# Performance work log

Hardware: AMD Instinct MI355X
Metric: run time of the kernel (lower is better)

## Reference

```python
import jax, jax.numpy as jnp
import numpy as np

WS = 7   # window_size
NH = 4   # num_heads


def setup_inputs() -> dict:
    key = jax.random.key(0)
    k0, k1 = jax.random.split(key, 2)
    dim = 384
    B, H, W = 8, 224, 224
    x = jax.random.normal(k0, (B, dim, H, W), dtype=jnp.float32)
    # torch nn.Linear stores weight as [out_features, in_features]
    qkv_w = jax.random.normal(k1, (3 * dim, dim), dtype=jnp.float32) * (dim ** -0.5)
    qkv_b = jnp.zeros((3 * dim,), dtype=jnp.float32)
    return {"x": x, "qkv_w": qkv_w, "qkv_b": qkv_b}


def reference(x, qkv_w, qkv_b):
    B, C, H, W = x.shape
    ws, nh = WS, NH
    hd = C // nh
    # NCHW -> NHWC
    x = jnp.transpose(x, (0, 2, 3, 1))
    pad_h = (-H) % ws
    pad_w = (-W) % ws
    x = jnp.pad(x, ((0, 0), (0, pad_h), (0, pad_w), (0, 0)))
    Hp, Wp = H + pad_h, W + pad_w
    # window partition -> [B*nWh*nWw, ws*ws, C]
    x = x.reshape(B, Hp // ws, ws, Wp // ws, ws, C)
    x = jnp.transpose(x, (0, 1, 3, 2, 4, 5)).reshape(-1, ws * ws, C)
    # QKV projection (torch Linear: x @ W.T + b)
    qkv = x @ qkv_w.T + qkv_b
    q, k, v = jnp.split(qkv, 3, axis=-1)

    def to_heads(t):  # [nW, ws*ws, C] -> [nW, nh, ws*ws, hd]
        return jnp.transpose(t.reshape(t.shape[0], ws * ws, nh, hd), (0, 2, 1, 3))

    q, k, v = to_heads(q), to_heads(k), to_heads(v)
    scale = jnp.asarray(hd, x.dtype) ** -0.5
    scores = jnp.einsum('wnqd,wnkd->wnqk', q * scale, k)
    attn = jax.nn.softmax(scores, axis=-1)
    out = jnp.einsum('wnqk,wnkd->wnqd', attn, v)
    # merge heads and reverse window partition
    out = jnp.transpose(out, (0, 2, 1, 3)).reshape(-1, ws * ws, C)
    out = out.reshape(B, Hp // ws, Wp // ws, ws, ws, C)
    out = jnp.transpose(out, (0, 1, 3, 2, 4, 5)).reshape(B, Hp, Wp, C)
    out = out[:, :H, :W, :]
    return jnp.transpose(out, (0, 3, 1, 2))
```

## Files before the change

kernel.cpp:

```cpp
#include <hip/hip_runtime.h>

typedef __attribute__((ext_vector_type(4))) float f32x4;
typedef __attribute__((ext_vector_type(8))) short s16x8;
typedef __attribute__((ext_vector_type(8))) unsigned short u16x8;

#define TOKS_PER_B 50176
#define CDIM 384
#define OCDIM 1152

__device__ __forceinline__ unsigned short f2bf(float f) {
  unsigned u = __builtin_bit_cast(unsigned, f);
  u += 0x7FFFu + ((u >> 16) & 1u);
  return (unsigned short)(u >> 16);
}
__device__ __forceinline__ unsigned cvt_pk(float lo, float hi) {
  unsigned r;
  asm("v_cvt_pk_bf16_f32 %0, %1, %2" : "=v"(r) : "v"(lo), "v"(hi));
  return r;
}

__global__ __launch_bounds__(256) void qkv_gemm(
    const float* __restrict__ x, const float* __restrict__ wq,
    const float* __restrict__ bias, unsigned short* __restrict__ qkv,
    long long t_base, int nwg) {
  __shared__ unsigned short As[128][32];
  __shared__ unsigned short Bs[128][32];
  const int tid  = threadIdx.x;
  const int lane = tid & 63, wv = tid >> 6;

  const int qq  = nwg >> 3, rr = nwg & 7;
  const int xcd = blockIdx.x & 7, pos = blockIdx.x >> 3;
  const int wgid = (xcd < rr ? xcd * (qq + 1) : rr * (qq + 1) + (xcd - rr) * qq) + pos;
  const int nb = wgid % 9, mb = wgid / 9;

  const long long t0 = t_base + (long long)mb * 128;
  const int b    = (int)(t0 / TOKS_PER_B);
  const int off0 = (int)(t0 - (long long)b * TOKS_PER_B);
  const float* xb = x + (size_t)b * CDIM * TOKS_PER_B + off0;
  const int n0 = nb * 128;
  const int ml = lane & 15, quad = lane >> 4;
  const int m_base = (wv & 1) * 64, n_base = (wv >> 1) * 64;

  const int tok  = tid & 127;
  const int kh   = (tid >> 7) << 4;
  const int keyA = (tok ^ (tok >> 2)) & 3;
  const int cA0  = kh >> 3;
  unsigned short* aw0 = &As[tok][((cA0 ^ keyA) << 3)];
  unsigned short* aw1 = &As[tok][(((cA0 + 1) ^ keyA) << 3)];
  const float* apk = xb + (size_t)kh * TOKS_PER_B + tok;

  const int bk4  = (tid & 7) * 4;
  const int bn   = tid >> 3;
  const int keyB = (bn ^ (bn >> 2)) & 3;
  const int bwoff = (((bk4 >> 3) ^ keyB) << 3) + (bk4 & 7);
  const float* wqp = wq + (size_t)(n0 + bn) * CDIM + bk4;

  const int keyR = (ml ^ (ml >> 2)) & 3;
  const int rq   = (quad ^ keyR) << 3;

  f32x4 acc[4][4] = {};

  for (int ks = 0; ks < 12; ++ks) {
    float va[16];
    #pragma unroll
    for (int i = 0; i < 16; ++i) va[i] = apk[(size_t)i * TOKS_PER_B];
    float4 vb[4];
    #pragma unroll
    for (int p = 0; p < 4; ++p) vb[p] = *(const float4*)(wqp + (size_t)p * 32 * CDIM);

    uint4 w;
    w.x = cvt_pk(va[0], va[1]);   w.y = cvt_pk(va[2], va[3]);
    w.z = cvt_pk(va[4], va[5]);   w.w = cvt_pk(va[6], va[7]);
    *(uint4*)aw0 = w;
    w.x = cvt_pk(va[8], va[9]);   w.y = cvt_pk(va[10], va[11]);
    w.z = cvt_pk(va[12], va[13]); w.w = cvt_pk(va[14], va[15]);
    *(uint4*)aw1 = w;
    #pragma unroll
    for (int p = 0; p < 4; ++p) {
      uint2 u;
      u.x = cvt_pk(vb[p].x, vb[p].y);
      u.y = cvt_pk(vb[p].z, vb[p].w);
      *(uint2*)&Bs[bn + p * 32][bwoff] = u;
    }
    __syncthreads();

    s16x8 af[4], bf[4];
    #pragma unroll
    for (int mi = 0; mi < 4; ++mi)
      af[mi] = __builtin_bit_cast(s16x8, *(const u16x8*)&As[m_base + mi * 16 + ml][rq]);
    #pragma unroll
    for (int ni = 0; ni < 4; ++ni)
      bf[ni] = __builtin_bit_cast(s16x8, *(const u16x8*)&Bs[n_base + ni * 16 + ml][rq]);
    #pragma unroll
    for (int mi = 0; mi < 4; ++mi)
      #pragma unroll
      for (int ni = 0; ni < 4; ++ni)
        acc[mi][ni] = __builtin_amdgcn_mfma_f32_16x16x32_bf16(af[mi], bf[ni], acc[mi][ni], 0, 0, 0);
    __syncthreads();

    apk += (size_t)32 * TOKS_PER_B;
    wqp += 32;
  }

  const long long mrow0 = (long long)mb * 128 + m_base;
  #pragma unroll
  for (int ni = 0; ni < 4; ++ni) {
    const int col = n0 + n_base + ni * 16 + ml;
    const float bv = bias[col];
    #pragma unroll
    for (int mi = 0; mi < 4; ++mi) {
      #pragma unroll
      for (int r = 0; r < 4; ++r) {
        const long long mrow = mrow0 + mi * 16 + quad * 4 + r;
        qkv[(size_t)mrow * OCDIM + col] = f2bf(acc[mi][ni][r] + bv);
      }
    }
  }
}

__global__ __launch_bounds__(64) void win_attn(
    const unsigned short* __restrict__ qkv, float* __restrict__ out,
    int win_base) {
  __shared__ unsigned short sh[64 * 72 + 96 * 72];
  unsigned short* P  = sh;
  unsigned short* Vt = sh + 64 * 72;
  const int lane = threadIdx.x;
  const int win  = win_base + blockIdx.x;
  const int head = blockIdx.y;
  const int b = win >> 10, hw = (win >> 5) & 31, ww = win & 31;
  const long long t00 = (long long)b * TOKS_PER_B + (long long)hw * 7 * 224 + ww * 7
                        - (long long)(win_base >> 5) * 1568;
  const unsigned short* base = qkv + t00 * OCDIM + head * 96;
  const int ml = lane & 15, quad = lane >> 4;

  for (int idx = lane; idx < 49 * 96; idx += 64) {
    const int pos = idx / 96, d = idx - pos * 96;
    const int r = pos / 7, cc = pos - r * 7;
    Vt[d * 72 + pos] = base[(size_t)(r * 224 + cc) * OCDIM + 768 + d];
  }
  for (int idx = lane; idx < 96 * 15; idx += 64) {
    const int d = idx / 15, j = 49 + (idx - d * 15);
    Vt[d * 72 + j] = 0;
  }

  s16x8 aq[4][3], bk[4][3];
  const s16x8 zf = {0, 0, 0, 0, 0, 0, 0, 0};
  #pragma unroll
  for (int mi = 0; mi < 4; ++mi) {
    const int pos = mi * 16 + ml;
    if (pos < 49) {
      const int r = pos / 7, cc = pos - r * 7;
      const unsigned short* rowp = base + (size_t)(r * 224 + cc) * OCDIM;
      #pragma unroll
      for (int ks = 0; ks < 3; ++ks) {
        aq[mi][ks] = __builtin_bit_cast(s16x8, *(const u16x8*)(rowp + ks * 32 + quad * 8));
        bk[mi][ks] = __builtin_bit_cast(s16x8, *(const u16x8*)(rowp + 384 + ks * 32 + quad * 8));
      }
    } else {
      #pragma unroll
      for (int ks = 0; ks < 3; ++ks) { aq[mi][ks] = zf; bk[mi][ks] = zf; }
    }
  }

  f32x4 sa[4][4] = {};
  #pragma unroll
  for (int ks = 0; ks < 3; ++ks)
    #pragma unroll
    for (int mi = 0; mi < 4; ++mi)
      #pragma unroll
      for (int ni = 0; ni < 4; ++ni)
        sa[mi][ni] = __builtin_amdgcn_mfma_f32_16x16x32_bf16(aq[mi][ks], bk[ni][ks], sa[mi][ni], 0, 0, 0);

  const float scale = 0.10206207261596577f;
  #pragma unroll
  for (int mi = 0; mi < 4; ++mi) {
    #pragma unroll
    for (int r = 0; r < 4; ++r) {
      float mx = -3.0e38f;
      #pragma unroll
      for (int ni = 0; ni < 4; ++ni)
        if (ni * 16 + ml < 49) mx = fmaxf(mx, sa[mi][ni][r]);
      mx = fmaxf(mx, __shfl_xor(mx, 1, 16));
      mx = fmaxf(mx, __shfl_xor(mx, 2, 16));
      mx = fmaxf(mx, __shfl_xor(mx, 4, 16));
      mx = fmaxf(mx, __shfl_xor(mx, 8, 16));
      float e[4], sum = 0.f;
      #pragma unroll
      for (int ni = 0; ni < 4; ++ni) {
        e[ni] = (ni * 16 + ml < 49) ? __expf((sa[mi][ni][r] - mx) * scale) : 0.f;
        sum += e[ni];
      }
      sum += __shfl_xor(sum, 1, 16);
      sum += __shfl_xor(sum, 2, 16);
      sum += __shfl_xor(sum, 4, 16);
      sum += __shfl_xor(sum, 8, 16);
      const float inv = 1.0f / sum;
      const int row = mi * 16 + quad * 4 + r;
      #pragma unroll
      for (int ni = 0; ni < 4; ++ni)
        P[row * 72 + ni * 16 + ml] = f2bf(e[ni] * inv);
    }
  }

  f32x4 oa[4][6] = {};
  #pragma unroll
  for (int ks = 0; ks < 2; ++ks) {
    s16x8 ap[4], bv[6];
    #pragma unroll
    for (int mi = 0; mi < 4; ++mi)
      ap[mi] = __builtin_bit_cast(s16x8, *(const u16x8*)&P[(mi * 16 + ml) * 72 + ks * 32 + quad * 8]);
    #pragma unroll
    for (int ni = 0; ni < 6; ++ni)
      bv[ni] = __builtin_bit_cast(s16x8, *(const u16x8*)&Vt[(ni * 16 + ml) * 72 + ks * 32 + quad * 8]);
    #pragma unroll
    for (int mi = 0; mi < 4; ++mi)
      #pragma unroll
      for (int ni = 0; ni < 6; ++ni)
        oa[mi][ni] = __builtin_amdgcn_mfma_f32_16x16x32_bf16(ap[mi], bv[ni], oa[mi][ni], 0, 0, 0);
  }

  float* O = (float*)sh;
  #pragma unroll
  for (int mi = 0; mi < 4; ++mi)
    #pragma unroll
    for (int r = 0; r < 4; ++r) {
      const int row = mi * 16 + quad * 4 + r;
      if (row < 49) {
        #pragma unroll
        for (int ni = 0; ni < 6; ++ni)
          O[row * 99 + ni * 16 + ml] = oa[mi][ni][r];
      }
    }
  const size_t obase = ((size_t)(b * CDIM + head * 96) * 224 + (size_t)hw * 7) * 224 + ww * 7;
  for (int idx = lane; idx < 49 * 96; idx += 64) {
    const int d = idx / 49, pos = idx - d * 49;
    const int r = pos / 7, cc = pos - r * 7;
    out[obase + ((size_t)d * 224 + r) * 224 + cc] = O[pos * 99 + d];
  }
}

extern "C" void kernel_launch(void* const* d_in, const int* in_sizes, int n_in,
                              void* d_out, int out_size, void* d_ws, size_t ws_size,
                              hipStream_t stream) {
  const float* x    = (const float*)d_in[0];
  const float* wq   = (const float*)d_in[1];
  const float* bias = (const float*)d_in[2];
  float* out = (float*)d_out;
  unsigned short* ws = (unsigned short*)d_ws;

  const long long UNIT_TOK = 6272;
  const size_t UNIT_BYTES = (size_t)UNIT_TOK * OCDIM * 2;
  int upc = (int)(ws_size / UNIT_BYTES);
  if (upc < 1) upc = 1;
  if (upc > 64) upc = 64;

  for (int u0 = 0; u0 < 64; u0 += upc) {
    const int units = (u0 + upc <= 64) ? upc : (64 - u0);
    const long long t_base = (long long)u0 * UNIT_TOK;
    const int toks = units * (int)UNIT_TOK;
    const int nwg = 9 * (toks / 128);
    qkv_gemm<<<dim3(nwg), dim3(256), 0, stream>>>(x, wq, bias, ws, t_base, nwg);
    dim3 g2(units * 128, 4);
    win_attn<<<g2, dim3(64), 0, stream>>>(ws, out, u0 * 128);
  }
}
```

Measured before the change: 2.549 ms.

## Write QKV directly in per-window-head layout with pre-transposed V

```diff
diff --git a/kernel.cpp b/kernel.cpp
--- a/kernel.cpp
+++ b/kernel.cpp
@@ -6,7 +6,11 @@
 
 #define TOKS_PER_B 50176
 #define CDIM 384
-#define OCDIM 1152
+
+#define REG_HW   15552
+#define QOFF     0
+#define KOFF     4704
+#define VTOFF    9408
 
 __device__ __forceinline__ unsigned short f2bf(float f) {
   unsigned u = __builtin_bit_cast(unsigned, f);
@@ -19,9 +23,20 @@
   return r;
 }
 
+__global__ __launch_bounds__(256) void pad_zero(unsigned short* __restrict__ ws, int total) {
+  const int i = blockIdx.x * 256 + threadIdx.x;
+  if (i >= total) return;
+  const int reg = i / 96, d = i - reg * 96;
+  unsigned short* p = ws + (size_t)reg * REG_HW + VTOFF + d * 64 + 49;
+  p[0] = 0;
+  unsigned* q = (unsigned*)(p + 1);
+  #pragma unroll
+  for (int j = 0; j < 7; ++j) q[j] = 0;
+}
+
 __global__ __launch_bounds__(256) void qkv_gemm(
     const float* __restrict__ x, const float* __restrict__ wq,
-    const float* __restrict__ bias, unsigned short* __restrict__ qkv,
+    const float* __restrict__ bias, unsigned short* __restrict__ ws,
     long long t_base, int nwg) {
   __shared__ unsigned short As[128][32];
   __shared__ unsigned short Bs[128][32];
@@ -29,8 +44,8 @@
   const int lane = tid & 63, wv = tid >> 6;
 
   const int qq  = nwg >> 3, rr = nwg & 7;
-  const int xcd = blockIdx.x & 7, pos = blockIdx.x >> 3;
-  const int wgid = (xcd < rr ? xcd * (qq + 1) : rr * (qq + 1) + (xcd - rr) * qq) + pos;
+  const int xcd = blockIdx.x & 7, posb = blockIdx.x >> 3;
+  const int wgid = (xcd < rr ? xcd * (qq + 1) : rr * (qq + 1) + (xcd - rr) * qq) + posb;
   const int nb = wgid % 9, mb = wgid / 9;
 
   const long long t0 = t_base + (long long)mb * 128;
@@ -41,135 +56,135 @@
   const int ml = lane & 15, quad = lane >> 4;
   const int m_base = (wv & 1) * 64, n_base = (wv >> 1) * 64;
 
-  const int tok  = tid & 127;
-  const int kh   = (tid >> 7) << 4;
-  const int keyA = (tok ^ (tok >> 2)) & 3;
-  const int cA0  = kh >> 3;
-  unsigned short* aw0 = &As[tok][((cA0 ^ keyA) << 3)];
-  unsigned short* aw1 = &As[tok][(((cA0 + 1) ^ keyA) << 3)];
-  const float* apk = xb + (size_t)kh * TOKS_PER_B + tok;
+  const int am   = tid & 31;
+  const int akq  = tid >> 5;
+  const int atok = am * 4;
+  const int aswr = (am >> 2) & 1;
+  const int awoff = (((akq >> 1) ^ (am & 3)) << 3) + (akq & 1) * 4;
+  const float* apk = xb + (size_t)(akq * 4) * TOKS_PER_B + atok;
 
   const int bk4  = (tid & 7) * 4;
   const int bn   = tid >> 3;
-  const int keyB = (bn ^ (bn >> 2)) & 3;
-  const int bwoff = (((bk4 >> 3) ^ keyB) << 3) + (bk4 & 7);
+  const int bswr = (bn >> 4) & 1;
+  const int bwoff = (((bk4 >> 3) ^ ((bn >> 2) & 3)) << 3) + (bk4 & 7);
   const float* wqp = wq + (size_t)(n0 + bn) * CDIM + bk4;
 
-  const int keyR = (ml ^ (ml >> 2)) & 3;
-  const int rq   = (quad ^ keyR) << 3;
+  const int rq = (quad ^ (ml >> 2)) << 3;
 
   f32x4 acc[4][4] = {};
+  f32x4 va[4]; f32x4 vb[4];
+  #pragma unroll
+  for (int p = 0; p < 4; ++p) va[p] = *(const f32x4*)(apk + (size_t)p * TOKS_PER_B);
+  #pragma unroll
+  for (int p = 0; p < 4; ++p) vb[p] = *(const f32x4*)(wqp + (size_t)p * 32 * CDIM);
 
   for (int ks = 0; ks < 12; ++ks) {
-    float va[16];
-    #pragma unroll
-    for (int i = 0; i < 16; ++i) va[i] = apk[(size_t)i * TOKS_PER_B];
-    float4 vb[4];
-    #pragma unroll
-    for (int p = 0; p < 4; ++p) vb[p] = *(const float4*)(wqp + (size_t)p * 32 * CDIM);
-
-    uint4 w;
-    w.x = cvt_pk(va[0], va[1]);   w.y = cvt_pk(va[2], va[3]);
-    w.z = cvt_pk(va[4], va[5]);   w.w = cvt_pk(va[6], va[7]);
-    *(uint4*)aw0 = w;
-    w.x = cvt_pk(va[8], va[9]);   w.y = cvt_pk(va[10], va[11]);
-    w.z = cvt_pk(va[12], va[13]); w.w = cvt_pk(va[14], va[15]);
-    *(uint4*)aw1 = w;
+    #pragma unroll
+    for (int t = 0; t < 4; ++t) {
+      uint2 u;
+      u.x = cvt_pk(va[0][t], va[1][t]);
+      u.y = cvt_pk(va[2][t], va[3][t]);
+      *(uint2*)&As[(atok + t) ^ aswr][awoff] = u;
+    }
     #pragma unroll
     for (int p = 0; p < 4; ++p) {
       uint2 u;
-      u.x = cvt_pk(vb[p].x, vb[p].y);
-      u.y = cvt_pk(vb[p].z, vb[p].w);
-      *(uint2*)&Bs[bn + p * 32][bwoff] = u;
+      u.x = cvt_pk(vb[p][0], vb[p][1]);
+      u.y = cvt_pk(vb[p][2], vb[p][3]);
+      *(uint2*)&Bs[(bn + 32 * p) ^ bswr][bwoff] = u;
     }
     __syncthreads();
-
+    if (ks < 11) {
+      apk += (size_t)32 * TOKS_PER_B;
+      wqp += 32;
+      #pragma unroll
+      for (int p = 0; p < 4; ++p) va[p] = *(const f32x4*)(apk + (size_t)p * TOKS_PER_B);
+      #pragma unroll
+      for (int p = 0; p < 4; ++p) vb[p] = *(const f32x4*)(wqp + (size_t)p * 32 * CDIM);
+    }
     s16x8 af[4], bf[4];
     #pragma unroll
     for (int mi = 0; mi < 4; ++mi)
-      af[mi] = __builtin_bit_cast(s16x8, *(const u16x8*)&As[m_base + mi * 16 + ml][rq]);
+      af[mi] = __builtin_bit_cast(s16x8, *(const u16x8*)&As[(m_base + mi * 16 + ml) ^ (mi & 1)][rq]);
     #pragma unroll
     for (int ni = 0; ni < 4; ++ni)
-      bf[ni] = __builtin_bit_cast(s16x8, *(const u16x8*)&Bs[n_base + ni * 16 + ml][rq]);
+      bf[ni] = __builtin_bit_cast(s16x8, *(const u16x8*)&Bs[(n_base + ni * 16 + ml) ^ (ni & 1)][rq]);
     #pragma unroll
     for (int mi = 0; mi < 4; ++mi)
       #pragma unroll
       for (int ni = 0; ni < 4; ++ni)
         acc[mi][ni] = __builtin_amdgcn_mfma_f32_16x16x32_bf16(af[mi], bf[ni], acc[mi][ni], 0, 0, 0);
     __syncthreads();
-
-    apk += (size_t)32 * TOKS_PER_B;
-    wqp += 32;
-  }
-
-  const long long mrow0 = (long long)mb * 128 + m_base;
+  }
+
+  int isV_[4]; size_t coff_[4]; float bv_[4];
   #pragma unroll
   for (int ni = 0; ni < 4; ++ni) {
-    const int col = n0 + n_base + ni * 16 + ml;
-    const float bv = bias[col];
+    const int colb = n0 + n_base + ni * 16;
+    const int sel  = colb / 384;
+    const int hd   = (colb - sel * 384) / 96;
+    const int db   = colb - sel * 384 - hd * 96;
+    bv_[ni]  = bias[colb + ml];
+    isV_[ni] = (sel == 2);
+    coff_[ni] = (size_t)hd * REG_HW +
+                (isV_[ni] ? (size_t)VTOFF + (size_t)(db + ml) * 64
+                          : (size_t)sel * 4704 + (size_t)(db + ml));
+  }
+  const unsigned tl00 = (unsigned)(mb * 128 + m_base + quad * 4);
+  #pragma unroll
+  for (int mi = 0; mi < 4; ++mi) {
+    #pragma unroll
+    for (int r = 0; r < 4; ++r) {
+      const unsigned tl = tl00 + mi * 16 + r;
+      const unsigned rl = tl / 224;
+      const unsigned cc = tl - rl * 224;
+      const unsigned wr = rl / 7, pr = rl - wr * 7;
+      const unsigned wc = cc / 7, pc = cc - wc * 7;
+      const size_t   wbase = (size_t)(wr * 32 + wc) * 4 * REG_HW;
+      const unsigned pos = pr * 7 + pc;
+      #pragma unroll
+      for (int ni = 0; ni < 4; ++ni) {
+        const unsigned short val = f2bf(acc[mi][ni][r] + bv_[ni]);
+        ws[wbase + coff_[ni] + (isV_[ni] ? (size_t)pos : (size_t)pos * 96)] = val;
+      }
+    }
+  }
+}
+
+__global__ __launch_bounds__(64) void win_attn(
+    const unsigned short* __restrict__ ws, float* __restrict__ out, int win_base) {
+  __shared__ float shraw[2450];
+  unsigned short* P = (unsigned short*)shraw;
+  float* O = shraw;
+  const int lane = threadIdx.x;
+  const int ml = lane & 15, quad = lane >> 4;
+  const int w = blockIdx.x, head = blockIdx.y;
+  const unsigned short* R = ws + (size_t)(w * 4 + head) * REG_HW;
+
+  const int gwin = win_base + w;
+  const int b = gwin >> 10, hw_ = (gwin >> 5) & 31, ww = gwin & 31;
+
+  const s16x8 zf = {0, 0, 0, 0, 0, 0, 0, 0};
+
+  f32x4 sa[4][4] = {};
+  #pragma unroll
+  for (int ks = 0; ks < 3; ++ks) {
+    s16x8 aq[4], bk[4];
     #pragma unroll
     for (int mi = 0; mi < 4; ++mi) {
-      #pragma unroll
-      for (int r = 0; r < 4; ++r) {
-        const long long mrow = mrow0 + mi * 16 + quad * 4 + r;
-        qkv[(size_t)mrow * OCDIM + col] = f2bf(acc[mi][ni][r] + bv);
-      }
-    }
-  }
-}
-
-__global__ __launch_bounds__(64) void win_attn(
-    const unsigned short* __restrict__ qkv, float* __restrict__ out,
-    int win_base) {
-  __shared__ unsigned short sh[64 * 72 + 96 * 72];
-  unsigned short* P  = sh;
-  unsigned short* Vt = sh + 64 * 72;
-  const int lane = threadIdx.x;
-  const int win  = win_base + blockIdx.x;
-  const int head = blockIdx.y;
-  const int b = win >> 10, hw = (win >> 5) & 31, ww = win & 31;
-  const long long t00 = (long long)b * TOKS_PER_B + (long long)hw * 7 * 224 + ww * 7
-                        - (long long)(win_base >> 5) * 1568;
-  const unsigned short* base = qkv + t00 * OCDIM + head * 96;
-  const int ml = lane & 15, quad = lane >> 4;
-
-  for (int idx = lane; idx < 49 * 96; idx += 64) {
-    const int pos = idx / 96, d = idx - pos * 96;
-    const int r = pos / 7, cc = pos - r * 7;
-    Vt[d * 72 + pos] = base[(size_t)(r * 224 + cc) * OCDIM + 768 + d];
-  }
-  for (int idx = lane; idx < 96 * 15; idx += 64) {
-    const int d = idx / 15, j = 49 + (idx - d * 15);
-    Vt[d * 72 + j] = 0;
-  }
-
-  s16x8 aq[4][3], bk[4][3];
-  const s16x8 zf = {0, 0, 0, 0, 0, 0, 0, 0};
-  #pragma unroll
-  for (int mi = 0; mi < 4; ++mi) {
-    const int pos = mi * 16 + ml;
-    if (pos < 49) {
-      const int r = pos / 7, cc = pos - r * 7;
-      const unsigned short* rowp = base + (size_t)(r * 224 + cc) * OCDIM;
-      #pragma unroll
-      for (int ks = 0; ks < 3; ++ks) {
-        aq[mi][ks] = __builtin_bit_cast(s16x8, *(const u16x8*)(rowp + ks * 32 + quad * 8));
-        bk[mi][ks] = __builtin_bit_cast(s16x8, *(const u16x8*)(rowp + 384 + ks * 32 + quad * 8));
-      }
-    } else {
-      #pragma unroll
-      for (int ks = 0; ks < 3; ++ks) { aq[mi][ks] = zf; bk[mi][ks] = zf; }
-    }
-  }
-
-  f32x4 sa[4][4] = {};
-  #pragma unroll
-  for (int ks = 0; ks < 3; ++ks)
-    #pragma unroll
-    for (int mi = 0; mi < 4; ++mi)
-      #pragma unroll
-      for (int ni = 0; ni < 4; ++ni)
-        sa[mi][ni] = __builtin_amdgcn_mfma_f32_16x16x32_bf16(aq[mi][ks], bk[ni][ks], sa[mi][ni], 0, 0, 0);
+      const int pos = mi * 16 + ml;
+      if (pos < 49) {
+        const unsigned short* rp = R + (size_t)pos * 96 + ks * 32 + quad * 8;
+        aq[mi] = __builtin_bit_cast(s16x8, *(const u16x8*)rp);
+        bk[mi] = __builtin_bit_cast(s16x8, *(const u16x8*)(rp + KOFF));
+      } else { aq[mi] = zf; bk[mi] = zf; }
+    }
+    #pragma unroll
+    for (int mi = 0; mi < 4; ++mi)
+      #pragma unroll
+      for (int ni = 0; ni < 4; ++ni)
+        sa[mi][ni] = __builtin_amdgcn_mfma_f32_16x16x32_bf16(aq[mi], bk[ni], sa[mi][ni], 0, 0, 0);
+  }
 
   const float scale = 0.10206207261596577f;
   #pragma unroll
@@ -202,40 +217,48 @@
     }
   }
 
-  f32x4 oa[4][6] = {};
-  #pragma unroll
-  for (int ks = 0; ks < 2; ++ks) {
-    s16x8 ap[4], bv[6];
-    #pragma unroll
-    for (int mi = 0; mi < 4; ++mi)
-      ap[mi] = __builtin_bit_cast(s16x8, *(const u16x8*)&P[(mi * 16 + ml) * 72 + ks * 32 + quad * 8]);
-    #pragma unroll
-    for (int ni = 0; ni < 6; ++ni)
-      bv[ni] = __builtin_bit_cast(s16x8, *(const u16x8*)&Vt[(ni * 16 + ml) * 72 + ks * 32 + quad * 8]);
-    #pragma unroll
-    for (int mi = 0; mi < 4; ++mi)
-      #pragma unroll
-      for (int ni = 0; ni < 6; ++ni)
-        oa[mi][ni] = __builtin_amdgcn_mfma_f32_16x16x32_bf16(ap[mi], bv[ni], oa[mi][ni], 0, 0, 0);
-  }
-
-  float* O = (float*)sh;
-  #pragma unroll
-  for (int mi = 0; mi < 4; ++mi)
-    #pragma unroll
-    for (int r = 0; r < 4; ++r) {
-      const int row = mi * 16 + quad * 4 + r;
-      if (row < 49) {
+  s16x8 ap[2][4];
+  #pragma unroll
+  for (int ks = 0; ks < 2; ++ks)
+    #pragma unroll
+    for (int mi = 0; mi < 4; ++mi)
+      ap[ks][mi] = __builtin_bit_cast(s16x8, *(const u16x8*)&P[(mi * 16 + ml) * 72 + ks * 32 + quad * 8]);
+
+  const unsigned short* Vt = R + VTOFF;
+  const size_t obase = ((size_t)(b * CDIM + head * 96) * 224 + (size_t)hw_ * 7) * 224 + ww * 7;
+
+  #pragma unroll
+  for (int hh = 0; hh < 2; ++hh) {
+    f32x4 oa[4][3] = {};
+    #pragma unroll
+    for (int ks = 0; ks < 2; ++ks) {
+      s16x8 bv[3];
+      #pragma unroll
+      for (int ni = 0; ni < 3; ++ni)
+        bv[ni] = __builtin_bit_cast(s16x8,
+            *(const u16x8*)(Vt + (size_t)(hh * 48 + ni * 16 + ml) * 64 + ks * 32 + quad * 8));
+      #pragma unroll
+      for (int mi = 0; mi < 4; ++mi)
         #pragma unroll
-        for (int ni = 0; ni < 6; ++ni)
-          O[row * 99 + ni * 16 + ml] = oa[mi][ni][r];
+        for (int ni = 0; ni < 3; ++ni)
+          oa[mi][ni] = __builtin_amdgcn_mfma_f32_16x16x32_bf16(ap[ks][mi], bv[ni], oa[mi][ni], 0, 0, 0);
+    }
+    #pragma unroll
+    for (int mi = 0; mi < 4; ++mi)
+      #pragma unroll
+      for (int r = 0; r < 4; ++r) {
+        const int row = mi * 16 + quad * 4 + r;
+        if (row < 49) {
+          #pragma unroll
+          for (int ni = 0; ni < 3; ++ni)
+            O[row * 50 + ni * 16 + ml] = oa[mi][ni][r];
+        }
       }
-    }
-  const size_t obase = ((size_t)(b * CDIM + head * 96) * 224 + (size_t)hw * 7) * 224 + ww * 7;
-  for (int idx = lane; idx < 49 * 96; idx += 64) {
-    const int d = idx / 49, pos = idx - d * 49;
-    const int r = pos / 7, cc = pos - r * 7;
-    out[obase + ((size_t)d * 224 + r) * 224 + cc] = O[pos * 99 + d];
+    for (int idx = lane; idx < 49 * 48; idx += 64) {
+      const int dd = idx / 49, pos = idx - dd * 49;
+      const int rr2 = pos / 7, cc2 = pos - rr2 * 7;
+      out[obase + ((size_t)(hh * 48 + dd) * 224 + rr2) * 224 + cc2] = O[pos * 50 + dd];
+    }
   }
 }
 
@@ -249,10 +272,15 @@
   unsigned short* ws = (unsigned short*)d_ws;
 
   const long long UNIT_TOK = 6272;
-  const size_t UNIT_BYTES = (size_t)UNIT_TOK * OCDIM * 2;
+  const size_t UNIT_BYTES = (size_t)128 * 4 * REG_HW * 2;
   int upc = (int)(ws_size / UNIT_BYTES);
   if (upc < 1) upc = 1;
   if (upc > 64) upc = 64;
+
+  {
+    const int total = upc * 128 * 4 * 96;
+    pad_zero<<<dim3((total + 255) / 256), dim3(256), 0, stream>>>(ws, total);
+  }
 
   for (int u0 = 0; u0 < 64; u0 += upc) {
     const int units = (u0 + upc <= 64) ? upc : (64 - u0);
```

Result: slower. 2.827 ms (+10.9%).
